# Kernel optimization log

Hardware: AMD Instinct MI355X
Metric: run time of the kernel (lower is better)

## Reference

```python
import jax, jax.numpy as jnp
import numpy as np

BEAM = 2  # groups

def setup_inputs() -> dict:
    key = jax.random.key(0)
    k1, k2, k3 = jax.random.split(key, 3)
    B, T, C, V = 16, 2048, 256, 2048
    z = jax.random.normal(k1, (B, T, C), jnp.float32)
    mask = jnp.ones((B, T, 1), jnp.float32)          # valid-position mask
    e = jax.random.normal(k2, (V, C), jnp.float32)   # codebook (rows 1: of embedding)
    advantages = jax.random.normal(k3, (B, BEAM), jnp.float32)  # scorer rewards (constants)
    return {"z": z, "mask": mask, "e": e, "advantages": advantages}

def reference(z, mask, e, advantages):
    B, T, C = z.shape
    V = e.shape[0]
    z_flat = z.reshape(-1, C)                                   # [B*T, C]
    logits = z_flat @ e.T                                       # cosine-sim scores [B*T, V]
    log_probs = jax.nn.log_softmax(logits, axis=-1).reshape(B, T, V)

    # --- batched, GPU-resident proxy for the per-sample CPU beam search:
    # top-BEAM token indices per timestep (beam 0 == argmax path, as used for VQ indexing)
    g_lp = jax.lax.stop_gradient(log_probs)
    _, idx = jax.lax.top_k(g_lp, BEAM)                          # [B, T, BEAM]
    sequences = jnp.transpose(idx, (0, 2, 1))                   # [B, BEAM, T]

    mask2 = mask[..., 0]                                        # [B, T]
    lengths = mask2.sum(axis=1)                                 # [B]

    # REINFORCE loss: gather per-token logps along V (no [B,BEAM,T,V] materialization)
    ptl = jnp.take_along_axis(log_probs, idx, axis=2)           # [B, T, BEAM]
    ptl = jnp.transpose(ptl, (0, 2, 1))                         # [B, BEAM, T]
    coef = jnp.exp(ptl - jax.lax.stop_gradient(ptl))            # == 1 in fwd; carries grad
    per_token_loss = -coef * advantages[:, :, None]             # [B, BEAM, T]
    per_b = (per_token_loss * mask2[:, None, :]).sum(axis=(1, 2)) / (BEAM * lengths)
    reinforce_loss = per_b.mean()

    # --- VQ indexing (one_hot @ e == gather rows of e)
    top_ind = sequences[:, 0]                                   # [B, T] best path
    z_q = e[top_ind]                                            # [B, T, C]

    # codebook usage histogram (scatter-add instead of dense one_hot)
    mflat = mask.reshape(-1)                                    # [B*T]
    e_mean = jnp.zeros((V,), z.dtype).at[top_ind.reshape(-1)].add(mflat) / mflat.sum()

    # --- masked losses
    valid = mask.sum() * C
    commitment_loss = (((z - jax.lax.stop_gradient(z_q)) ** 2) * mask).sum() / valid
    smoothness_loss = (((z[:, :-1, :] - z[:, 1:, :]) ** 2) * mask[:, 1:, :]).sum() / valid

    # straight-through
    z_q_st = (z_flat + jax.lax.stop_gradient(z_q.reshape(-1, C) - z_flat)).reshape(B, T, C) * mask
    return (log_probs, z_q_st, smoothness_loss, commitment_loss, reinforce_loss, e_mean)
```

## Files before the change

kernel.cpp:

```cpp
#include <hip/hip_runtime.h>
#include <hip/hip_bf16.h>

#define BT_ROWS 32768
#define CDIM    256
#define VDIM    2048
#define TDIM    2048
#define EHL_HALF (VDIM * CDIM)

typedef __attribute__((ext_vector_type(4))) float f32x4;
typedef __attribute__((ext_vector_type(8))) short s16x8;

__device__ __forceinline__ ushort bf16_rne(float v) {
    uint u = __float_as_uint(v);
    uint r = u + 0x7FFFu + ((u >> 16) & 1u);
    return (ushort)(r >> 16);
}
__device__ __forceinline__ float bf16_to_f(ushort h) {
    return __uint_as_float(((uint)h) << 16);
}

__global__ void kp_econv(const float* __restrict__ e, ushort* __restrict__ ehl)
{
    const int s   = blockIdx.x * 256 + threadIdx.x;
    const int col = s >> 5;
    const int kg  = s & 31;
    const int ks  = kg >> 2;
    const int lane = (kg & 3) * 16 + (col & 15);
    const int cbg = col >> 4;
    const float4 v0 = *(const float4*)&e[col * CDIM + kg * 8];
    const float4 v1 = *(const float4*)&e[col * CDIM + kg * 8 + 4];
    float vv[8] = {v0.x, v0.y, v0.z, v0.w, v1.x, v1.y, v1.z, v1.w};
    ushort h[8], l[8];
    #pragma unroll
    for (int j = 0; j < 8; ++j) {
        h[j] = bf16_rne(vv[j]);
        l[j] = bf16_rne(vv[j] - bf16_to_f(h[j]));
    }
    const int off = ((cbg * 8 + ks) * 64 + lane) * 8;
    uint4 hp, lp_;
    hp.x = h[0] | ((uint)h[1] << 16); hp.y = h[2] | ((uint)h[3] << 16);
    hp.z = h[4] | ((uint)h[5] << 16); hp.w = h[6] | ((uint)h[7] << 16);
    lp_.x = l[0] | ((uint)l[1] << 16); lp_.y = l[2] | ((uint)l[3] << 16);
    lp_.z = l[4] | ((uint)l[5] << 16); lp_.w = l[6] | ((uint)l[7] << 16);
    *(uint4*)&ehl[off] = hp;
    *(uint4*)&ehl[EHL_HALF + off] = lp_;
}

__global__ __launch_bounds__(256, 2)
void k1_gemm_lse(const float* __restrict__ z, const ushort* __restrict__ ehl,
                 float* __restrict__ lp, float* __restrict__ ls_arr,
                 int* __restrict__ amax_arr)
{
    __shared__ __align__(16) ushort zsm[2 * 4 * 8 * 64 * 8];
    __shared__ float smx[256], ssm[256];
    __shared__ int   sam[256];

    const int tid  = threadIdx.x;
    const int w    = tid >> 6;
    const int l    = tid & 63;
    const int lg   = l >> 4;
    const int li   = l & 15;
    const int row0 = blockIdx.x * 64;

    smx[tid] = -3.0e38f; ssm[tid] = 0.f; sam[tid] = 0;

    #pragma unroll
    for (int p = 0; p < 8; ++p) {
        const int s    = p * 256 + tid;
        const int rbks = s >> 6;
        const int lane = s & 63;
        const int row  = (rbks >> 3) * 16 + (lane & 15);
        const int kg   = (rbks & 7) * 4 + (lane >> 4);
        const float4 v0 = *(const float4*)&z[(size_t)(row0 + row) * CDIM + kg * 8];
        const float4 v1 = *(const float4*)&z[(size_t)(row0 + row) * CDIM + kg * 8 + 4];
        float vv[8] = {v0.x, v0.y, v0.z, v0.w, v1.x, v1.y, v1.z, v1.w};
        ushort h[8], lo[8];
        #pragma unroll
        for (int j = 0; j < 8; ++j) {
            h[j]  = bf16_rne(vv[j]);
            lo[j] = bf16_rne(vv[j] - bf16_to_f(h[j]));
        }
        const int off = (rbks * 64 + lane) * 8;
        uint4 hp, lq;
        hp.x = h[0] | ((uint)h[1] << 16); hp.y = h[2] | ((uint)h[3] << 16);
        hp.z = h[4] | ((uint)h[5] << 16); hp.w = h[6] | ((uint)h[7] << 16);
        lq.x = lo[0] | ((uint)lo[1] << 16); lq.y = lo[2] | ((uint)lo[3] << 16);
        lq.z = lo[4] | ((uint)lo[5] << 16); lq.w = lo[6] | ((uint)lo[7] << 16);
        *(uint4*)&zsm[off] = hp;
        *(uint4*)&zsm[16384 + off] = lq;
    }
    __syncthreads();

    const ushort* eh = ehl;
    const ushort* el = ehl + EHL_HALF;

    for (int chunk = 0; chunk < 4; ++chunk) {
        const int col0 = chunk * 512 + w * 128;
        const int cbg0 = col0 >> 4;
        f32x4 acc[4][8];
        #pragma unroll
        for (int rb = 0; rb < 4; ++rb)
            #pragma unroll
            for (int cb = 0; cb < 8; ++cb) acc[rb][cb] = (f32x4)0.f;

        #pragma unroll
        for (int ks = 0; ks < 8; ++ks) {
            s16x8 ah[4], al[4];
            #pragma unroll
            for (int rb = 0; rb < 4; ++rb) {
                ah[rb] = *(const s16x8*)&zsm[((rb * 8 + ks) * 64 + l) * 8];
                al[rb] = *(const s16x8*)&zsm[16384 + ((rb * 8 + ks) * 64 + l) * 8];
            }
            #pragma unroll
            for (int cb = 0; cb < 8; ++cb) {
                const s16x8 bh = *(const s16x8*)&eh[(((cbg0 + cb) * 8 + ks) * 64 + l) * 8];
                const s16x8 bl = *(const s16x8*)&el[(((cbg0 + cb) * 8 + ks) * 64 + l) * 8];
                #pragma unroll
                for (int rb = 0; rb < 4; ++rb) {
                    acc[rb][cb] = __builtin_amdgcn_mfma_f32_16x16x32_bf16(ah[rb], bh, acc[rb][cb], 0, 0, 0);
                    acc[rb][cb] = __builtin_amdgcn_mfma_f32_16x16x32_bf16(ah[rb], bl, acc[rb][cb], 0, 0, 0);
                    acc[rb][cb] = __builtin_amdgcn_mfma_f32_16x16x32_bf16(al[rb], bh, acc[rb][cb], 0, 0, 0);
                }
            }
        }

        #pragma unroll
        for (int rb = 0; rb < 4; ++rb)
            #pragma unroll
            for (int cb = 0; cb < 8; ++cb)
                #pragma unroll
                for (int r = 0; r < 4; ++r)
                    lp[(size_t)(row0 + rb * 16 + lg * 4 + r) * VDIM + col0 + cb * 16 + li] = acc[rb][cb][r];

        #pragma unroll
        for (int rb = 0; rb < 4; ++rb) {
            float rm[4]; int ri[4];
            #pragma unroll
            for (int r = 0; r < 4; ++r) { rm[r] = acc[rb][0][r]; ri[r] = col0 + li; }
            #pragma unroll
            for (int cb = 1; cb < 8; ++cb)
                #pragma unroll
                for (int r = 0; r < 4; ++r) {
                    const float v = acc[rb][cb][r];
                    if (v > rm[r]) { rm[r] = v; ri[r] = col0 + cb * 16 + li; }
                }
            #pragma unroll
            for (int mk = 1; mk < 16; mk <<= 1)
                #pragma unroll
                for (int r = 0; r < 4; ++r) {
                    const float ov = __shfl_xor(rm[r], mk);
                    const int   oi = __shfl_xor(ri[r], mk);
                    if (ov > rm[r] || (ov == rm[r] && oi < ri[r])) { rm[r] = ov; ri[r] = oi; }
                }
            float se[4] = {0.f, 0.f, 0.f, 0.f};
            #pragma unroll
            for (int cb = 0; cb < 8; ++cb)
                #pragma unroll
                for (int r = 0; r < 4; ++r) se[r] += __expf(acc[rb][cb][r] - rm[r]);
            #pragma unroll
            for (int mk = 1; mk < 16; mk <<= 1)
                #pragma unroll
                for (int r = 0; r < 4; ++r) se[r] += __shfl_xor(se[r], mk);
            if (li == 0) {
                #pragma unroll
                for (int r = 0; r < 4; ++r) {
                    const int sr = w * 64 + rb * 16 + lg * 4 + r;
                    const float mo = smx[sr], so = ssm[sr];
                    const float mn = fmaxf(mo, rm[r]);
                    ssm[sr] = so * __expf(mo - mn) + se[r] * __expf(rm[r] - mn);
                    smx[sr] = mn;
                    if (rm[r] > mo) sam[sr] = ri[r];
                }
            }
        }
    }

    __syncthreads();
    if (tid < 64) {
        const int row = tid;
        float m = smx[row]; int a = sam[row];
        #pragma unroll
        for (int ww = 1; ww < 4; ++ww) {
            const float mw = smx[ww * 64 + row];
            const int   aw = sam[ww * 64 + row];
            if (mw > m) { m = mw; a = aw; }
            else if (mw == m && aw < a) { a = aw; }
        }
        float s = 0.f;
        #pragma unroll
        for (int ww = 0; ww < 4; ++ww) s += ssm[ww * 64 + row] * expf(smx[ww * 64 + row] - m);
        ls_arr[row0 + row]   = m + logf(s);
        amax_arr[row0 + row] = a;
    }
}

__global__ void k2_norm(float* __restrict__ lp, const float* __restrict__ ls)
{
    const int n4 = (BT_ROWS * VDIM) / 4;
    int idx = blockIdx.x * blockDim.x + threadIdx.x;
    const int stride = gridDim.x * blockDim.x;
    float4* p = (float4*)lp;
    for (; idx < n4; idx += stride) {
        float lsv = ls[idx >> 9];
        float4 v = p[idx];
        v.x -= lsv; v.y -= lsv; v.z -= lsv; v.w -= lsv;
        p[idx] = v;
    }
}

__global__ void k0_zero(float* __restrict__ ha)
{
    int i = blockIdx.x * blockDim.x + threadIdx.x;
    if (i < VDIM + 3) ha[i] = 0.f;
}

__global__ __launch_bounds__(256)
void k3_small(const float* __restrict__ z, const float* __restrict__ mask,
              const float* __restrict__ e, const int* __restrict__ amax,
              float* __restrict__ zq, float* __restrict__ hist,
              float* __restrict__ accum)
{
    const int tid = threadIdx.x;
    const int rbase = blockIdx.x * 32;
    float commit = 0.f, smooth = 0.f, mksum = 0.f;
    for (int rr = 0; rr < 32; ++rr) {
        const int row = rbase + rr;
        const int t = row & (TDIM - 1);
        const float mk = mask[row];
        const int a = amax[row];
        const float zv = z[(size_t)row * CDIM + tid];
        const float qa = e[(size_t)a * CDIM + tid];
        const float d = zv - qa;
        commit += d * d * mk;
        if (t > 0) {
            const float zp = z[(size_t)(row - 1) * CDIM + tid];
            const float dd = zv - zp;
            smooth += dd * dd * mk;
        }
        zq[(size_t)row * CDIM + tid] = qa * mk;
        if (tid == 0) { atomicAdd(&hist[a], mk); mksum += mk; }
    }
    #pragma unroll
    for (int off = 1; off < 64; off <<= 1) {
        commit += __shfl_xor(commit, off);
        smooth += __shfl_xor(smooth, off);
    }
    __shared__ float red[8];
    const int lane = tid & 63, wid = tid >> 6;
    if (lane == 0) { red[wid] = commit; red[4 + wid] = smooth; }
    __syncthreads();
    if (tid == 0) {
        atomicAdd(&accum[1], red[0] + red[1] + red[2] + red[3]);
        atomicAdd(&accum[2], red[4] + red[5] + red[6] + red[7]);
        atomicAdd(&accum[0], mksum);
    }
}

__global__ void k4_final(const float* __restrict__ adv, const float* __restrict__ hist,
                         const float* __restrict__ accum, float* __restrict__ sc,
                         float* __restrict__ emean)
{
    const float msum = accum[0];
    for (int v = threadIdx.x; v < VDIM; v += 256) emean[v] = hist[v] / msum;
    if (threadIdx.x == 0) {
        const float denom = msum * (float)CDIM;
        sc[0] = accum[2] / denom;
        sc[1] = accum[1] / denom;
        float sa = 0.f;
        for (int k = 0; k < 32; ++k) sa += adv[k];
        sc[2] = -sa / 32.f;
    }
}

extern "C" void kernel_launch(void* const* d_in, const int* in_sizes, int n_in,
                              void* d_out, int out_size, void* d_ws, size_t ws_size,
                              hipStream_t stream)
{
    const float* z    = (const float*)d_in[0];
    const float* mask = (const float*)d_in[1];
    const float* e    = (const float*)d_in[2];
    const float* adv  = (const float*)d_in[3];

    float* lp    = (float*)d_out;
    float* zq    = lp + (size_t)BT_ROWS * VDIM;
    float* sc    = zq + (size_t)BT_ROWS * CDIM;
    float* emean = sc + 3;

    ushort* ehl = (ushort*)zq;

    float* ls    = (float*)d_ws;
    int*   amax  = (int*)((float*)d_ws + BT_ROWS);
    float* hist  = (float*)d_ws + 2 * BT_ROWS;
    float* accum = hist + VDIM;

    k0_zero    <<<9,    256, 0, stream>>>(hist);
    kp_econv   <<<256,  256, 0, stream>>>(e, ehl);
    k1_gemm_lse<<<512,  256, 0, stream>>>(z, ehl, lp, ls, amax);
    k2_norm    <<<2048, 256, 0, stream>>>(lp, ls);
    k3_small   <<<1024, 256, 0, stream>>>(z, mask, e, amax, zq, hist, accum);
    k4_final   <<<1,    256, 0, stream>>>(adv, hist, accum, sc, emean);
}
```

Measured before the change: 636.8 us.

## Halve GEMM row tile, swap MFMA operands for vector stores, raise occupancy

The GEMM+LSE kernel now handles 32 rows per block instead of 64, launches 1024 blocks, and sets launch bounds to 4 waves per SIMD. The MFMA operands are swapped (codebook as A, z as B), so each lane holds 4 consecutive columns of one row. That allows float4 stores of logits and a per-lane row reduction over the xor-16/32 shuffles. The intent is more occupancy, fewer accumulator registers and coalesced vector stores. In exchange, each block re-reads the codebook for half as many rows, which doubles global/L2 traffic on the e operand.

After: 804.7 us. 26.4% more time.

```diff
diff --git a/kernel.cpp b/kernel.cpp
--- a/kernel.cpp
+++ b/kernel.cpp
@@ -46,26 +46,26 @@
     *(uint4*)&ehl[EHL_HALF + off] = lp_;
 }
 
-__global__ __launch_bounds__(256, 2)
+__global__ __launch_bounds__(256, 4)
 void k1_gemm_lse(const float* __restrict__ z, const ushort* __restrict__ ehl,
                  float* __restrict__ lp, float* __restrict__ ls_arr,
                  int* __restrict__ amax_arr)
 {
-    __shared__ __align__(16) ushort zsm[2 * 4 * 8 * 64 * 8];
-    __shared__ float smx[256], ssm[256];
-    __shared__ int   sam[256];
+    __shared__ __align__(16) ushort zsm[2 * 2 * 8 * 64 * 8];
+    __shared__ float smx[128], ssm[128];
+    __shared__ int   sam[128];
 
     const int tid  = threadIdx.x;
     const int w    = tid >> 6;
     const int l    = tid & 63;
     const int lg   = l >> 4;
     const int li   = l & 15;
-    const int row0 = blockIdx.x * 64;
-
-    smx[tid] = -3.0e38f; ssm[tid] = 0.f; sam[tid] = 0;
+    const int row0 = blockIdx.x * 32;
+
+    if (tid < 128) { smx[tid] = -3.0e38f; ssm[tid] = 0.f; sam[tid] = 0; }
 
     #pragma unroll
-    for (int p = 0; p < 8; ++p) {
+    for (int p = 0; p < 4; ++p) {
         const int s    = p * 256 + tid;
         const int rbks = s >> 6;
         const int lane = s & 63;
@@ -87,7 +87,7 @@
         lq.x = lo[0] | ((uint)lo[1] << 16); lq.y = lo[2] | ((uint)lo[3] << 16);
         lq.z = lo[4] | ((uint)lo[5] << 16); lq.w = lo[6] | ((uint)lo[7] << 16);
         *(uint4*)&zsm[off] = hp;
-        *(uint4*)&zsm[16384 + off] = lq;
+        *(uint4*)&zsm[8192 + off] = lq;
     }
     __syncthreads();
 
@@ -97,98 +97,89 @@
     for (int chunk = 0; chunk < 4; ++chunk) {
         const int col0 = chunk * 512 + w * 128;
         const int cbg0 = col0 >> 4;
-        f32x4 acc[4][8];
-        #pragma unroll
-        for (int rb = 0; rb < 4; ++rb)
+        f32x4 acc[2][8];
+        #pragma unroll
+        for (int rb = 0; rb < 2; ++rb)
             #pragma unroll
             for (int cb = 0; cb < 8; ++cb) acc[rb][cb] = (f32x4)0.f;
 
         #pragma unroll
         for (int ks = 0; ks < 8; ++ks) {
-            s16x8 ah[4], al[4];
-            #pragma unroll
-            for (int rb = 0; rb < 4; ++rb) {
-                ah[rb] = *(const s16x8*)&zsm[((rb * 8 + ks) * 64 + l) * 8];
-                al[rb] = *(const s16x8*)&zsm[16384 + ((rb * 8 + ks) * 64 + l) * 8];
+            s16x8 zbh[2], zbl[2];
+            #pragma unroll
+            for (int rb = 0; rb < 2; ++rb) {
+                zbh[rb] = *(const s16x8*)&zsm[((rb * 8 + ks) * 64 + l) * 8];
+                zbl[rb] = *(const s16x8*)&zsm[8192 + ((rb * 8 + ks) * 64 + l) * 8];
             }
             #pragma unroll
             for (int cb = 0; cb < 8; ++cb) {
-                const s16x8 bh = *(const s16x8*)&eh[(((cbg0 + cb) * 8 + ks) * 64 + l) * 8];
-                const s16x8 bl = *(const s16x8*)&el[(((cbg0 + cb) * 8 + ks) * 64 + l) * 8];
+                const s16x8 eah = *(const s16x8*)&eh[(((cbg0 + cb) * 8 + ks) * 64 + l) * 8];
+                const s16x8 eal = *(const s16x8*)&el[(((cbg0 + cb) * 8 + ks) * 64 + l) * 8];
                 #pragma unroll
-                for (int rb = 0; rb < 4; ++rb) {
-                    acc[rb][cb] = __builtin_amdgcn_mfma_f32_16x16x32_bf16(ah[rb], bh, acc[rb][cb], 0, 0, 0);
-                    acc[rb][cb] = __builtin_amdgcn_mfma_f32_16x16x32_bf16(ah[rb], bl, acc[rb][cb], 0, 0, 0);
-                    acc[rb][cb] = __builtin_amdgcn_mfma_f32_16x16x32_bf16(al[rb], bh, acc[rb][cb], 0, 0, 0);
+                for (int rb = 0; rb < 2; ++rb) {
+                    acc[rb][cb] = __builtin_amdgcn_mfma_f32_16x16x32_bf16(eah, zbh[rb], acc[rb][cb], 0, 0, 0);
+                    acc[rb][cb] = __builtin_amdgcn_mfma_f32_16x16x32_bf16(eah, zbl[rb], acc[rb][cb], 0, 0, 0);
+                    acc[rb][cb] = __builtin_amdgcn_mfma_f32_16x16x32_bf16(eal, zbh[rb], acc[rb][cb], 0, 0, 0);
                 }
             }
         }
 
         #pragma unroll
-        for (int rb = 0; rb < 4; ++rb)
+        for (int rb = 0; rb < 2; ++rb)
             #pragma unroll
             for (int cb = 0; cb < 8; ++cb)
-                #pragma unroll
-                for (int r = 0; r < 4; ++r)
-                    lp[(size_t)(row0 + rb * 16 + lg * 4 + r) * VDIM + col0 + cb * 16 + li] = acc[rb][cb][r];
-
-        #pragma unroll
-        for (int rb = 0; rb < 4; ++rb) {
-            float rm[4]; int ri[4];
-            #pragma unroll
-            for (int r = 0; r < 4; ++r) { rm[r] = acc[rb][0][r]; ri[r] = col0 + li; }
-            #pragma unroll
-            for (int cb = 1; cb < 8; ++cb)
+                *(f32x4*)&lp[(size_t)(row0 + rb * 16 + li) * VDIM + col0 + cb * 16 + lg * 4] = acc[rb][cb];
+
+        #pragma unroll
+        for (int rb = 0; rb < 2; ++rb) {
+            float rm = acc[rb][0][0];
+            int   ri = col0 + lg * 4;
+            #pragma unroll
+            for (int cb = 0; cb < 8; ++cb)
                 #pragma unroll
                 for (int r = 0; r < 4; ++r) {
                     const float v = acc[rb][cb][r];
-                    if (v > rm[r]) { rm[r] = v; ri[r] = col0 + cb * 16 + li; }
+                    const int idx = col0 + cb * 16 + lg * 4 + r;
+                    if (v > rm) { rm = v; ri = idx; }
                 }
             #pragma unroll
-            for (int mk = 1; mk < 16; mk <<= 1)
-                #pragma unroll
-                for (int r = 0; r < 4; ++r) {
-                    const float ov = __shfl_xor(rm[r], mk);
-                    const int   oi = __shfl_xor(ri[r], mk);
-                    if (ov > rm[r] || (ov == rm[r] && oi < ri[r])) { rm[r] = ov; ri[r] = oi; }
-                }
-            float se[4] = {0.f, 0.f, 0.f, 0.f};
+            for (int mk = 16; mk < 64; mk <<= 1) {
+                const float ov = __shfl_xor(rm, mk);
+                const int   oi = __shfl_xor(ri, mk);
+                if (ov > rm || (ov == rm && oi < ri)) { rm = ov; ri = oi; }
+            }
+            float se = 0.f;
             #pragma unroll
             for (int cb = 0; cb < 8; ++cb)
                 #pragma unroll
-                for (int r = 0; r < 4; ++r) se[r] += __expf(acc[rb][cb][r] - rm[r]);
-            #pragma unroll
-            for (int mk = 1; mk < 16; mk <<= 1)
-                #pragma unroll
-                for (int r = 0; r < 4; ++r) se[r] += __shfl_xor(se[r], mk);
-            if (li == 0) {
-                #pragma unroll
-                for (int r = 0; r < 4; ++r) {
-                    const int sr = w * 64 + rb * 16 + lg * 4 + r;
-                    const float mo = smx[sr], so = ssm[sr];
-                    const float mn = fmaxf(mo, rm[r]);
-                    ssm[sr] = so * __expf(mo - mn) + se[r] * __expf(rm[r] - mn);
-                    smx[sr] = mn;
-                    if (rm[r] > mo) sam[sr] = ri[r];
-                }
+                for (int r = 0; r < 4; ++r) se += __expf(acc[rb][cb][r] - rm);
+            #pragma unroll
+            for (int mk = 16; mk < 64; mk <<= 1) se += __shfl_xor(se, mk);
+            if (l < 16) {
+                const int sr = w * 32 + rb * 16 + li;
+                const float mo = smx[sr], so = ssm[sr];
+                const float mn = fmaxf(mo, rm);
+                ssm[sr] = so * __expf(mo - mn) + se * __expf(rm - mn);
+                smx[sr] = mn;
+                if (rm > mo) sam[sr] = ri;
             }
         }
     }
 
     __syncthreads();
-    if (tid < 64) {
+    if (tid < 32) {
         const int row = tid;
         float m = smx[row]; int a = sam[row];
         #pragma unroll
         for (int ww = 1; ww < 4; ++ww) {
-            const float mw = smx[ww * 64 + row];
-            const int   aw = sam[ww * 64 + row];
+            const float mw = smx[ww * 32 + row];
+            const int   aw = sam[ww * 32 + row];
             if (mw > m) { m = mw; a = aw; }
             else if (mw == m && aw < a) { a = aw; }
         }
         float s = 0.f;
         #pragma unroll
-        for (int ww = 0; ww < 4; ++ww) s += ssm[ww * 64 + row] * expf(smx[ww * 64 + row] - m);
+        for (int ww = 0; ww < 4; ++ww) s += ssm[ww * 32 + row] * expf(smx[ww * 32 + row] - m);
         ls_arr[row0 + row]   = m + logf(s);
         amax_arr[row0 + row] = a;
     }
@@ -295,7 +286,7 @@
 
     k0_zero    <<<9,    256, 0, stream>>>(hist);
     kp_econv   <<<256,  256, 0, stream>>>(e, ehl);
-    k1_gemm_lse<<<512,  256, 0, stream>>>(z, ehl, lp, ls, amax);
+    k1_gemm_lse<<<1024, 256, 0, stream>>>(z, ehl, lp, ls, amax);
     k2_norm    <<<2048, 256, 0, stream>>>(lp, ls);
     k3_small   <<<1024, 256, 0, stream>>>(z, mask, e, amax, zq, hist, accum);
     k4_final   <<<1,    256, 0, stream>>>(adv, hist, accum, sc, emean);
```
